# Optimization experiments

Measured on AMD Instinct MI355X. Metric: run time of the kernel, lower is better.

Reference implementation:

```python
import jax, jax.numpy as jnp
import numpy as np

N, F_IN, HID, HEADS, NC, E, NG = 50000, 128, 64, 4, 8, 800000, 512


def setup_inputs() -> dict:
    key = jax.random.key(0)
    ks = jax.random.split(key, 16)
    x = jax.random.normal(ks[0], (N, F_IN), dtype=jnp.float32)
    # edges with src != dst so every node's incoming set is exactly {neighbors, self-loop}
    dst = jax.random.randint(ks[1], (E,), 0, N, dtype=jnp.int64)
    off = jax.random.randint(ks[2], (E,), 1, N, dtype=jnp.int64)
    src = (dst + off) % N
    edge_index = jnp.stack([src, dst])
    batch = jnp.sort(jax.random.randint(ks[3], (N,), 0, NG, dtype=jnp.int64))
    g = 1.0 / np.sqrt(F_IN)
    W1 = jax.random.uniform(ks[4], (F_IN, HEADS * HID), jnp.float32, -g, g)
    att_src1 = jax.random.normal(ks[5], (HEADS, HID), jnp.float32) * 0.1
    att_dst1 = jax.random.normal(ks[6], (HEADS, HID), jnp.float32) * 0.1
    b1 = jnp.zeros((HEADS * HID,), jnp.float32)
    g2 = 1.0 / np.sqrt(HEADS * HID)
    W2 = jax.random.uniform(ks[7], (HEADS * HID, HID), jnp.float32, -g2, g2)
    att_src2 = jax.random.normal(ks[8], (1, HID), jnp.float32) * 0.1
    att_dst2 = jax.random.normal(ks[9], (1, HID), jnp.float32) * 0.1
    b2 = jnp.zeros((HID,), jnp.float32)
    g3 = 1.0 / np.sqrt(HID)
    lin_w = jax.random.uniform(ks[10], (HID, NC), jnp.float32, -g3, g3)
    lin_b = jnp.zeros((NC,), jnp.float32)
    return dict(x=x, edge_index=edge_index, batch=batch, W1=W1, att_src1=att_src1,
                att_dst1=att_dst1, b1=b1, W2=W2, att_src2=att_src2, att_dst2=att_dst2,
                b2=b2, lin_w=lin_w, lin_b=lin_b)


def gat_layer(x, src, dst, W, att_s, att_d, bias, heads, out_ch):
    # PyG GATConv: h = x @ W, e_ij = LeakyReLU(a_s.h_j + a_d.h_i), softmax over dst groups
    h = (x @ W).reshape(-1, heads, out_ch)                    # [N,H,C]
    a_s = jnp.einsum('nhc,hc->nh', h, att_s)                  # [N,H]
    a_d = jnp.einsum('nhc,hc->nh', h, att_d)
    e = jax.nn.leaky_relu(a_s[src] + a_d[dst], 0.2)           # [Ef,H]
    m = jax.ops.segment_max(e, dst, num_segments=N)           # stable segment softmax
    ex = jnp.exp(e - m[dst])
    s = jax.ops.segment_sum(ex, dst, num_segments=N)
    alpha = ex / (s[dst] + 1e-16)                             # [Ef,H]
    msg = h[src] * alpha[:, :, None]                          # [Ef,H,C]
    out = jax.ops.segment_sum(msg, dst, num_segments=N)       # [N,H,C]
    return out.reshape(-1, heads * out_ch) + bias, alpha


def reference(x, edge_index, batch, W1, att_src1, att_dst1, b1,
              W2, att_src2, att_dst2, b2, lin_w, lin_b):
    loops = jnp.arange(N, dtype=edge_index.dtype)
    src = jnp.concatenate([edge_index[0], loops])             # add self-loops (PyG default)
    dst = jnp.concatenate([edge_index[1], loops])
    h, alpha1 = gat_layer(x, src, dst, W1, att_src1, att_dst1, b1, HEADS, HID)
    h = jax.nn.relu(h)
    # conv2 on edge_index_1 (already has self-loops; PyG remove+add is a no-op here)
    h, alpha2 = gat_layer(h, src, dst, W2, att_src2, att_dst2, b2, 1, HID)
    h = jax.nn.relu(h)
    sums = jax.ops.segment_sum(h, batch, num_segments=NG)     # global_mean_pool
    cnt = jax.ops.segment_sum(jnp.ones((N,), h.dtype), batch, num_segments=NG)
    pooled = sums / jnp.maximum(cnt, 1.0)[:, None]
    # dropout is identity in eval mode
    return pooled @ lin_w + lin_b
```

## Files before the change

kernel.cpp:

```cpp
#include <hip/hip_runtime.h>

#define F_IN 128
#define HID 64
#define HEADS 4
#define NC 8

typedef __bf16 bf16_t;
typedef bf16_t bf16x8 __attribute__((ext_vector_type(8)));
typedef float f32x4 __attribute__((ext_vector_type(4)));

union BF8 { bf16x8 v; ushort u[8]; };


__device__ __forceinline__ ushort f2bf(float f) {
    uint u = __float_as_uint(f);
    return (ushort)((u + 0x7fffu + ((u >> 16) & 1u)) >> 16);
}
__device__ __forceinline__ float bf2f(ushort h) {
    return __uint_as_float(((uint)h) << 16);
}
__device__ __forceinline__ float edgew(float e) {
    e = (e > 0.f) ? e : 0.2f * e;
    return __expf(e);
}

__global__ void k_setup(const float* __restrict__ W1, const float* __restrict__ W2,
                        ushort* __restrict__ w1hi, ushort* __restrict__ w1lo,
                        ushort* __restrict__ w2hi, ushort* __restrict__ w2lo,
                        int* __restrict__ deg, int N, int* __restrict__ counts, int NG) {
    int i = blockIdx.x * blockDim.x + threadIdx.x;
    if (i < N) deg[i] = 1;
    if (i < NG) counts[i] = 0;
    if (i < 128 * 256) {
        int k = i >> 8, n = i & 255;
        int cy = n >> 7, ct = (n >> 4) & 7, c = n & 15, kc = k >> 5, ls = (k >> 3) & 3, j = k & 7;
        size_t off = ((((size_t)cy * 8 + ct) * 4 + kc) * 64 + (ls * 16 + c)) * 8 + j;
        float w = W1[i];
        ushort hi = f2bf(w);
        w1hi[off] = hi; w1lo[off] = f2bf(w - bf2f(hi));
    }
    if (i < 256 * 64) {
        int k = i >> 6, n = i & 63;
        int ct = n >> 4, c = n & 15, kc = k >> 5, ls = (k >> 3) & 3, j = k & 7;
        size_t off = (((size_t)ct * 8 + kc) * 64 + (ls * 16 + c)) * 8 + j;
        float w = W2[i];
        ushort hi = f2bf(w);
        w2hi[off] = hi; w2lo[off] = f2bf(w - bf2f(hi));
    }
}

__global__ void k_count(const int* __restrict__ ei, int E, int* __restrict__ deg,
                        const int* __restrict__ batch, int N, int* __restrict__ counts) {
    int i = blockIdx.x * blockDim.x + threadIdx.x;
    if (i < E) atomicAdd(&deg[ei[E + i]], 1);
    if (i < N) atomicAdd(&counts[batch[i]], 1);
}

__global__ __launch_bounds__(1024) void k_scan_part(const int* __restrict__ v,
                                                    int* __restrict__ excl,
                                                    int* __restrict__ bsum, int n) {
    __shared__ int buf[1024];
    int tid = threadIdx.x;
    int i = blockIdx.x * 1024 + tid;
    int val = (i < n) ? v[i] : 0;
    buf[tid] = val;
    __syncthreads();
    for (int off = 1; off < 1024; off <<= 1) {
        int t = (tid >= off) ? buf[tid - off] : 0;
        __syncthreads();
        buf[tid] += t;
        __syncthreads();
    }
    if (i < n) excl[i] = buf[tid] - val;
    if (tid == 1023) bsum[blockIdx.x] = buf[1023];
}

__global__ __launch_bounds__(1024) void k_scan_small2(const int* __restrict__ bsum,
                                                      int* __restrict__ boff, int nb,
                                                      int* __restrict__ total_out,
                                                      const int* __restrict__ counts,
                                                      int* __restrict__ gstart, int ng) {
    __shared__ int buf[1024];
    int tid = threadIdx.x;
    const int* src = (blockIdx.x == 0) ? bsum : counts;
    int cnt = (blockIdx.x == 0) ? nb : ng;
    int val = (tid < cnt) ? src[tid] : 0;
    buf[tid] = val;
    __syncthreads();
    for (int off = 1; off < 1024; off <<= 1) {
        int t = (tid >= off) ? buf[tid - off] : 0;
        __syncthreads();
        buf[tid] += t;
        __syncthreads();
    }
    if (blockIdx.x == 0) {
        if (tid < cnt) boff[tid] = buf[tid] - val;
        if (tid == 1023) total_out[0] = buf[1023];
    } else {
        if (tid < cnt) gstart[tid] = buf[tid] - val;
        if (tid == 1023) gstart[ng] = buf[1023];
    }
}

__global__ void k_scan_add_self(int* __restrict__ rowstart, const int* __restrict__ boff,
                                int* __restrict__ cursor, int* __restrict__ csr, int n) {
    int i = blockIdx.x * blockDim.x + threadIdx.x;
    if (i < n) {
        int rs = rowstart[i] + boff[i >> 10];
        rowstart[i] = rs;
        csr[rs] = i;
        cursor[i] = 1;
    }
}

__global__ void k_scatter(const int* __restrict__ ei, int E, const int* __restrict__ rowstart,
                          int* __restrict__ cursor, int* __restrict__ csr) {
    int e = blockIdx.x * blockDim.x + threadIdx.x;
    if (e < E) {
        int d = ei[E + e], s = ei[e];
        int pos = atomicAdd(&cursor[d], 1);
        csr[rowstart[d] + pos] = s;
    }
}

__global__ __launch_bounds__(256) void k_gemm1(const float* __restrict__ x,
                                               const ushort* __restrict__ w1hi,
                                               const ushort* __restrict__ w1lo,
                                               const float* __restrict__ atts,
                                               const float* __restrict__ attd,
                                               ushort* __restrict__ h1b,
                                               float* __restrict__ as1, float* __restrict__ ad1,
                                               int N) {
    __shared__ __align__(16) ushort lhi[16384];
    __shared__ __align__(16) ushort llo[16384];
    int tid = threadIdx.x;
    int cy = blockIdx.y;
    {
        float4* dh = (float4*)lhi; const float4* sh = (const float4*)(w1hi + (size_t)cy * 16384);
        float4* dl = (float4*)llo; const float4* sl = (const float4*)(w1lo + (size_t)cy * 16384);
        #pragma unroll
        for (int i = 0; i < 8; i++) {
            dh[tid + i * 256] = sh[tid + i * 256];
            dl[tid + i * 256] = sl[tid + i * 256];
        }
    }
    __syncthreads();
    int w = tid >> 6, l = tid & 63;
    int lc = l & 15, lk = l >> 4;
    int rbase = blockIdx.x * 256 + w * 64;

    f32x4 acc[4][8];
    #pragma unroll
    for (int mt = 0; mt < 4; mt++)
        #pragma unroll
        for (int ct = 0; ct < 8; ct++) acc[mt][ct] = (f32x4){0.f, 0.f, 0.f, 0.f};

    #pragma unroll
    for (int kc = 0; kc < 4; kc++) {
        BF8 ahi[4], alo[4];
        #pragma unroll
        for (int mt = 0; mt < 4; mt++) {
            int row = rbase + mt * 16 + lc;
            float4 v0 = {0.f, 0.f, 0.f, 0.f}, v1 = v0;
            if (row < N) {
                const float* xp = x + (size_t)row * F_IN + kc * 32 + lk * 8;
                v0 = *(const float4*)xp; v1 = *(const float4*)(xp + 4);
            }
            float vals[8] = {v0.x, v0.y, v0.z, v0.w, v1.x, v1.y, v1.z, v1.w};
            #pragma unroll
            for (int j = 0; j < 8; j++) {
                ushort h = f2bf(vals[j]);
                ahi[mt].u[j] = h;
                alo[mt].u[j] = f2bf(vals[j] - bf2f(h));
            }
        }
        #pragma unroll
        for (int ct = 0; ct < 8; ct++) {
            int boff = ((ct * 4 + kc) * 64 + l) * 8;
            bf16x8 bhi = *(const bf16x8*)(lhi + boff);
            bf16x8 blo = *(const bf16x8*)(llo + boff);
            #pragma unroll
            for (int mt = 0; mt < 4; mt++) {
                acc[mt][ct] = __builtin_amdgcn_mfma_f32_16x16x32_bf16(ahi[mt].v, bhi, acc[mt][ct], 0, 0, 0);
                acc[mt][ct] = __builtin_amdgcn_mfma_f32_16x16x32_bf16(alo[mt].v, bhi, acc[mt][ct], 0, 0, 0);
                acc[mt][ct] = __builtin_amdgcn_mfma_f32_16x16x32_bf16(ahi[mt].v, blo, acc[mt][ct], 0, 0, 0);
            }
        }
    }
    #pragma unroll
    for (int mt = 0; mt < 4; mt++) {
        int rowb = rbase + mt * 16 + lk * 4;
        #pragma unroll
        for (int ct = 0; ct < 8; ct++) {
            int col = cy * 128 + ct * 16 + lc;
            #pragma unroll
            for (int r = 0; r < 4; r++) {
                int row = rowb + r;
                if (row < N) h1b[(size_t)row * 256 + col] = f2bf(acc[mt][ct][r]);
            }
        }
        #pragma unroll
        for (int hh = 0; hh < 2; hh++) {
            float s[4] = {0.f, 0.f, 0.f, 0.f}, d[4] = {0.f, 0.f, 0.f, 0.f};
            #pragma unroll
            for (int cq = 0; cq < 4; cq++) {
                int ct = hh * 4 + cq;
                int col = cy * 128 + ct * 16 + lc;
                float av = atts[col], dv = attd[col];
                #pragma unroll
                for (int r = 0; r < 4; r++) { s[r] += acc[mt][ct][r] * av; d[r] += acc[mt][ct][r] * dv; }
            }
            #pragma unroll
            for (int r = 0; r < 4; r++) {
                #pragma unroll
                for (int off = 1; off < 16; off <<= 1) {
                    s[r] += __shfl_xor(s[r], off);
                    d[r] += __shfl_xor(d[r], off);
                }
            }
            if (lc == 0) {
                int head = cy * 2 + hh;
                #pragma unroll
                for (int r = 0; r < 4; r++) {
                    int row = rowb + r;
                    if (row < N) { as1[row * 4 + head] = s[r]; ad1[row * 4 + head] = d[r]; }
                }
            }
        }
    }
}

__global__ __launch_bounds__(256) void k_gemm2(const ushort* __restrict__ xin,
                                               const ushort* __restrict__ w2hi,
                                               const ushort* __restrict__ w2lo,
                                               const float* __restrict__ atts,
                                               const float* __restrict__ attd,
                                               ushort* __restrict__ h2b,
                                               float* __restrict__ as2, float* __restrict__ ad2,
                                               int N) {
    __shared__ __align__(16) ushort lhi[16384];
    __shared__ __align__(16) ushort llo[16384];
    int tid = threadIdx.x;
    {
        float4* dh = (float4*)lhi; const float4* sh = (const float4*)w2hi;
        float4* dl = (float4*)llo; const float4* sl = (const float4*)w2lo;
        #pragma unroll
        for (int i = 0; i < 8; i++) {
            dh[tid + i * 256] = sh[tid + i * 256];
            dl[tid + i * 256] = sl[tid + i * 256];
        }
    }
    __syncthreads();
    int w = tid >> 6, l = tid & 63;
    int lc = l & 15, lk = l >> 4;
    int rbase = blockIdx.x * 256 + w * 64;

    f32x4 acc[4][4];
    #pragma unroll
    for (int mt = 0; mt < 4; mt++)
        #pragma unroll
        for (int ct = 0; ct < 4; ct++) acc[mt][ct] = (f32x4){0.f, 0.f, 0.f, 0.f};

    #pragma unroll
    for (int kc = 0; kc < 8; kc++) {
        BF8 a[4];
        #pragma unroll
        for (int mt = 0; mt < 4; mt++) {
            int row = rbase + mt * 16 + lc;
            if (row < N) {
                a[mt].v = *(const bf16x8*)(xin + (size_t)row * 256 + kc * 32 + lk * 8);
            } else {
                #pragma unroll
                for (int j = 0; j < 8; j++) a[mt].u[j] = 0;
            }
        }
        #pragma unroll
        for (int ct = 0; ct < 4; ct++) {
            int boff = ((ct * 8 + kc) * 64 + l) * 8;
            bf16x8 bhi = *(const bf16x8*)(lhi + boff);
            bf16x8 blo = *(const bf16x8*)(llo + boff);
            #pragma unroll
            for (int mt = 0; mt < 4; mt++) {
                acc[mt][ct] = __builtin_amdgcn_mfma_f32_16x16x32_bf16(a[mt].v, bhi, acc[mt][ct], 0, 0, 0);
                acc[mt][ct] = __builtin_amdgcn_mfma_f32_16x16x32_bf16(a[mt].v, blo, acc[mt][ct], 0, 0, 0);
            }
        }
    }
    #pragma unroll
    for (int mt = 0; mt < 4; mt++) {
        int rowb = rbase + mt * 16 + lk * 4;
        #pragma unroll
        for (int ct = 0; ct < 4; ct++) {
            int col = ct * 16 + lc;
            #pragma unroll
            for (int r = 0; r < 4; r++) {
                int row = rowb + r;
                if (row < N) h2b[(size_t)row * 64 + col] = f2bf(acc[mt][ct][r]);
            }
        }
        float s[4] = {0.f, 0.f, 0.f, 0.f}, d[4] = {0.f, 0.f, 0.f, 0.f};
        #pragma unroll
        for (int ct = 0; ct < 4; ct++) {
            int col = ct * 16 + lc;
            float av = atts[col], dv = attd[col];
            #pragma unroll
            for (int r = 0; r < 4; r++) { s[r] += acc[mt][ct][r] * av; d[r] += acc[mt][ct][r] * dv; }
        }
        #pragma unroll
        for (int r = 0; r < 4; r++) {
            #pragma unroll
            for (int off = 1; off < 16; off <<= 1) {
                s[r] += __shfl_xor(s[r], off);
                d[r] += __shfl_xor(d[r], off);
            }
        }
        if (lc == 0) {
            #pragma unroll
            for (int r = 0; r < 4; r++) {
                int row = rowb + r;
                if (row < N) { as2[row] = s[r]; ad2[row] = d[r]; }
            }
        }
    }
}


__global__ __launch_bounds__(256) void k_agg1(const ushort* __restrict__ h1b,
                                              const float* __restrict__ as, const float* __restrict__ ad,
                                              const int* __restrict__ rowstart, const int* __restrict__ csr,
                                              const float* __restrict__ b1,
                                              ushort* __restrict__ out1b, int N) {
    int n = blockIdx.x * 4 + (threadIdx.x >> 6);
    int lane = threadIdx.x & 63;
    if (n >= N) return;
    int head = lane >> 4;
    int coff = lane * 4;
    float adv = ad[n * 4 + head];
    int beg = rowstart[n], end = rowstart[n + 1];
    float a0 = 0.f, a1 = 0.f, a2 = 0.f, a3 = 0.f, ssum = 0.f;
    int j = beg;
    for (; j + 8 <= end; j += 8) {
        int s[8];
        #pragma unroll
        for (int i = 0; i < 8; i++) s[i] = csr[j + i];
        float e[8];
        #pragma unroll
        for (int i = 0; i < 8; i++) e[i] = as[s[i] * 4 + head];
        ushort4 hv[8];
        #pragma unroll
        for (int i = 0; i < 8; i++) hv[i] = *(const ushort4*)(h1b + (size_t)s[i] * 256 + coff);
        #pragma unroll
        for (int i = 0; i < 8; i++) {
            float wv = edgew(e[i] + adv);
            ssum += wv;
            a0 += wv * bf2f(hv[i].x); a1 += wv * bf2f(hv[i].y);
            a2 += wv * bf2f(hv[i].z); a3 += wv * bf2f(hv[i].w);
        }
    }
    for (; j < end; j++) {
        int s0 = csr[j];
        float wv = edgew(as[s0 * 4 + head] + adv);
        ushort4 v0 = *(const ushort4*)(h1b + (size_t)s0 * 256 + coff);
        ssum += wv;
        a0 += wv * bf2f(v0.x); a1 += wv * bf2f(v0.y);
        a2 += wv * bf2f(v0.z); a3 += wv * bf2f(v0.w);
    }
    float inv = 1.f / ssum;
    float o0 = fmaxf(a0 * inv + b1[coff + 0], 0.f);
    float o1 = fmaxf(a1 * inv + b1[coff + 1], 0.f);
    float o2 = fmaxf(a2 * inv + b1[coff + 2], 0.f);
    float o3 = fmaxf(a3 * inv + b1[coff + 3], 0.f);
    ushort4 o;
    o.x = f2bf(o0); o.y = f2bf(o1); o.z = f2bf(o2); o.w = f2bf(o3);
    *(ushort4*)(out1b + (size_t)n * 256 + coff) = o;
}

__global__ __launch_bounds__(256) void k_agg2(const ushort* __restrict__ h2b,
                                              const float* __restrict__ as, const float* __restrict__ ad,
                                              const int* __restrict__ rowstart, const int* __restrict__ csr,
                                              const float* __restrict__ b2,
                                              float* __restrict__ out2, int N) {
    int n = blockIdx.x * 4 + (threadIdx.x >> 6);
    int lane = threadIdx.x & 63;
    if (n >= N) return;
    float adv = ad[n];
    int beg = rowstart[n], end = rowstart[n + 1];
    float acc = 0.f, ssum = 0.f;
    int j = beg;
    for (; j + 8 <= end; j += 8) {
        int s[8];
        #pragma unroll
        for (int i = 0; i < 8; i++) s[i] = csr[j + i];
        float e[8];
        #pragma unroll
        for (int i = 0; i < 8; i++) e[i] = as[s[i]];
        ushort hv[8];
        #pragma unroll
        for (int i = 0; i < 8; i++) hv[i] = h2b[(size_t)s[i] * 64 + lane];
        #pragma unroll
        for (int i = 0; i < 8; i++) {
            float wv = edgew(e[i] + adv);
            ssum += wv;
            acc += wv * bf2f(hv[i]);
        }
    }
    for (; j < end; j++) {
        int s0 = csr[j];
        float wv = edgew(as[s0] + adv);
        ssum += wv;
        acc += wv * bf2f(h2b[(size_t)s0 * 64 + lane]);
    }
    float o = acc / ssum + b2[lane];
    out2[(size_t)n * 64 + lane] = o > 0.f ? o : 0.f;
}


__global__ __launch_bounds__(64) void k_pool(const float* __restrict__ out2,
                                             const int* __restrict__ gstart,
                                             const float* __restrict__ lin_w,
                                             const float* __restrict__ lin_b,
                                             float* __restrict__ out, int NG) {
    __shared__ float mean[64];
    int g = blockIdx.x;
    int lane = threadIdx.x;
    int beg = gstart[g], end = gstart[g + 1];
    float s = 0.f;
    for (int n = beg; n < end; n++) s += out2[(size_t)n * 64 + lane];
    float cnt = (float)(end - beg);
    mean[lane] = s / fmaxf(cnt, 1.f);
    __syncthreads();
    if (lane < NC) {
        float acc = lin_b[lane];
        #pragma unroll
        for (int c = 0; c < 64; c++) acc += mean[c] * lin_w[c * NC + lane];
        out[g * NC + lane] = acc;
    }
}


extern "C" void kernel_launch(void* const* d_in, const int* in_sizes, int n_in,
                              void* d_out, int out_size, void* d_ws, size_t ws_size,
                              hipStream_t stream) {
    const float* x      = (const float*)d_in[0];
    const int*   ei     = (const int*)d_in[1];
    const int*   batch  = (const int*)d_in[2];
    const float* W1     = (const float*)d_in[3];
    const float* att_s1 = (const float*)d_in[4];
    const float* att_d1 = (const float*)d_in[5];
    const float* b1     = (const float*)d_in[6];
    const float* W2     = (const float*)d_in[7];
    const float* att_s2 = (const float*)d_in[8];
    const float* att_d2 = (const float*)d_in[9];
    const float* b2     = (const float*)d_in[10];
    const float* lin_w  = (const float*)d_in[11];
    const float* lin_b  = (const float*)d_in[12];
    float* out = (float*)d_out;

    const int N  = in_sizes[0] / F_IN;
    const int E  = in_sizes[1] / 2;
    const int NG = out_size / NC;
    const int NE = E + N;
    const int NB = (N + 1023) / 1024;

    char* p = (char*)d_ws;
    auto alloc = [&](size_t bytes) { char* r = p; p += (bytes + 255) & ~(size_t)255; return r; };
    ushort* h1b     = (ushort*)alloc(sizeof(ushort) * (size_t)N * 256);
    ushort* out1b   = (ushort*)alloc(sizeof(ushort) * (size_t)N * 256);
    ushort* h2b     = (ushort*)alloc(sizeof(ushort) * (size_t)N * 64);
    float*  out2    = (float*)alloc(sizeof(float) * (size_t)N * 64);
    float*  as1     = (float*)alloc(sizeof(float) * (size_t)N * 4);
    float*  ad1     = (float*)alloc(sizeof(float) * (size_t)N * 4);
    float*  as2     = (float*)alloc(sizeof(float) * (size_t)N);
    float*  ad2     = (float*)alloc(sizeof(float) * (size_t)N);
    int*    rowstart= (int*)alloc(sizeof(int) * (size_t)(N + 1));
    int*    itmp    = (int*)alloc(sizeof(int) * (size_t)N);
    int*    csr     = (int*)alloc(sizeof(int) * (size_t)NE);
    int*    counts  = (int*)alloc(sizeof(int) * (size_t)NG);
    int*    gstart  = (int*)alloc(sizeof(int) * (size_t)(NG + 1));
    int*    bsum    = (int*)alloc(sizeof(int) * 1024);
    int*    boff    = (int*)alloc(sizeof(int) * 1024);
    ushort* w1hi    = (ushort*)alloc(sizeof(ushort) * 32768);
    ushort* w1lo    = (ushort*)alloc(sizeof(ushort) * 32768);
    ushort* w2hi    = (ushort*)alloc(sizeof(ushort) * 16384);
    ushort* w2lo    = (ushort*)alloc(sizeof(ushort) * 16384);

    int bs = 256;
    k_setup<<<(N + bs - 1) / bs, bs, 0, stream>>>(W1, W2, w1hi, w1lo, w2hi, w2lo,
                                                  itmp, N, counts, NG);
    k_count<<<(E + bs - 1) / bs, bs, 0, stream>>>(ei, E, itmp, batch, N, counts);
    k_scan_part<<<NB, 1024, 0, stream>>>(itmp, rowstart, bsum, N);
    k_scan_small2<<<2, 1024, 0, stream>>>(bsum, boff, NB, rowstart + N, counts, gstart, NG);
    k_scan_add_self<<<(N + 1023) / 1024, 1024, 0, stream>>>(rowstart, boff, itmp, csr, N);
    k_scatter<<<(E + bs - 1) / bs, bs, 0, stream>>>(ei, E, rowstart, itmp, csr);

    k_gemm1<<<dim3((N + 255) / 256, 2), 256, 0, stream>>>(x, w1hi, w1lo, att_s1, att_d1, h1b, as1, ad1, N);
    k_agg1<<<(N + 3) / 4, 256, 0, stream>>>(h1b, as1, ad1, rowstart, csr, b1, out1b, N);

    k_gemm2<<<(N + 255) / 256, 256, 0, stream>>>(out1b, w2hi, w2lo, att_s2, att_d2, h2b, as2, ad2, N);
    k_agg2<<<(N + 3) / 4, 256, 0, stream>>>(h2b, as2, ad2, rowstart, csr, b2, out2, N);

    k_pool<<<NG, 64, 0, stream>>>(out2, gstart, lin_w, lin_b, out, NG);
}
```

Baseline: 321.4 us.

## Drop W1 low-part GEMM term and restructure aggregation to edge-parallel staging

Layer-1 GEMM no longer computes the bf16 low-part correction for W1, which removes one of three MFMAs per tile along with half the weight LDS traffic. Both aggregation kernels are rewritten so each wave computes edge weights for 64 edges in parallel, stages them in shared memory, and then gathers neighbour features with 16-byte loads, splitting edges across lane groups and combining the partial sums with shuffles. The aim is more memory-level parallelism and wider loads in the gather-bound aggregation. It costs some GEMM1 accuracy and relies on wave-level implicit synchronisation when reading the shared staging arrays without a barrier.

```diff
diff --git a/kernel.cpp b/kernel.cpp
--- a/kernel.cpp
+++ b/kernel.cpp
@@ -25,7 +25,7 @@
 }
 
 __global__ void k_setup(const float* __restrict__ W1, const float* __restrict__ W2,
-                        ushort* __restrict__ w1hi, ushort* __restrict__ w1lo,
+                        ushort* __restrict__ w1hi,
                         ushort* __restrict__ w2hi, ushort* __restrict__ w2lo,
                         int* __restrict__ deg, int N, int* __restrict__ counts, int NG) {
     int i = blockIdx.x * blockDim.x + threadIdx.x;
@@ -35,9 +35,7 @@
         int k = i >> 8, n = i & 255;
         int cy = n >> 7, ct = (n >> 4) & 7, c = n & 15, kc = k >> 5, ls = (k >> 3) & 3, j = k & 7;
         size_t off = ((((size_t)cy * 8 + ct) * 4 + kc) * 64 + (ls * 16 + c)) * 8 + j;
-        float w = W1[i];
-        ushort hi = f2bf(w);
-        w1hi[off] = hi; w1lo[off] = f2bf(w - bf2f(hi));
+        w1hi[off] = f2bf(W1[i]);
     }
     if (i < 256 * 64) {
         int k = i >> 6, n = i & 63;
@@ -125,24 +123,18 @@
 
 __global__ __launch_bounds__(256) void k_gemm1(const float* __restrict__ x,
                                                const ushort* __restrict__ w1hi,
-                                               const ushort* __restrict__ w1lo,
                                                const float* __restrict__ atts,
                                                const float* __restrict__ attd,
                                                ushort* __restrict__ h1b,
                                                float* __restrict__ as1, float* __restrict__ ad1,
                                                int N) {
     __shared__ __align__(16) ushort lhi[16384];
-    __shared__ __align__(16) ushort llo[16384];
     int tid = threadIdx.x;
     int cy = blockIdx.y;
     {
         float4* dh = (float4*)lhi; const float4* sh = (const float4*)(w1hi + (size_t)cy * 16384);
-        float4* dl = (float4*)llo; const float4* sl = (const float4*)(w1lo + (size_t)cy * 16384);
-        #pragma unroll
-        for (int i = 0; i < 8; i++) {
-            dh[tid + i * 256] = sh[tid + i * 256];
-            dl[tid + i * 256] = sl[tid + i * 256];
-        }
+        #pragma unroll
+        for (int i = 0; i < 8; i++) dh[tid + i * 256] = sh[tid + i * 256];
     }
     __syncthreads();
     int w = tid >> 6, l = tid & 63;
@@ -178,12 +170,10 @@
         for (int ct = 0; ct < 8; ct++) {
             int boff = ((ct * 4 + kc) * 64 + l) * 8;
             bf16x8 bhi = *(const bf16x8*)(lhi + boff);
-            bf16x8 blo = *(const bf16x8*)(llo + boff);
             #pragma unroll
             for (int mt = 0; mt < 4; mt++) {
                 acc[mt][ct] = __builtin_amdgcn_mfma_f32_16x16x32_bf16(ahi[mt].v, bhi, acc[mt][ct], 0, 0, 0);
                 acc[mt][ct] = __builtin_amdgcn_mfma_f32_16x16x32_bf16(alo[mt].v, bhi, acc[mt][ct], 0, 0, 0);
-                acc[mt][ct] = __builtin_amdgcn_mfma_f32_16x16x32_bf16(ahi[mt].v, blo, acc[mt][ct], 0, 0, 0);
             }
         }
     }
@@ -324,94 +314,165 @@
     }
 }
 
-
-__global__ __launch_bounds__(256) void k_agg1(const ushort* __restrict__ h1b,
-                                              const float* __restrict__ as, const float* __restrict__ ad,
-                                              const int* __restrict__ rowstart, const int* __restrict__ csr,
-                                              const float* __restrict__ b1,
-                                              ushort* __restrict__ out1b, int N) {
-    int n = blockIdx.x * 4 + (threadIdx.x >> 6);
-    int lane = threadIdx.x & 63;
+__global__ __launch_bounds__(256) void k_fagg1(const ushort* __restrict__ h1b,
+                                               const float* __restrict__ as1,
+                                               const float* __restrict__ ad1,
+                                               const int* __restrict__ rowstart,
+                                               const int* __restrict__ csr,
+                                               const float* __restrict__ b1,
+                                               ushort* __restrict__ out1b, int N) {
+    __shared__ float lw[4][256];
+    __shared__ int   lsrc[4][64];
+    int wid = threadIdx.x >> 6, lane = threadIdx.x & 63;
+    int n = blockIdx.x * 4 + wid;
     if (n >= N) return;
-    int head = lane >> 4;
-    int coff = lane * 4;
-    float adv = ad[n * 4 + head];
     int beg = rowstart[n], end = rowstart[n + 1];
-    float a0 = 0.f, a1 = 0.f, a2 = 0.f, a3 = 0.f, ssum = 0.f;
-    int j = beg;
-    for (; j + 8 <= end; j += 8) {
-        int s[8];
-        #pragma unroll
-        for (int i = 0; i < 8; i++) s[i] = csr[j + i];
-        float e[8];
-        #pragma unroll
-        for (int i = 0; i < 8; i++) e[i] = as[s[i] * 4 + head];
-        ushort4 hv[8];
-        #pragma unroll
-        for (int i = 0; i < 8; i++) hv[i] = *(const ushort4*)(h1b + (size_t)s[i] * 256 + coff);
-        #pragma unroll
-        for (int i = 0; i < 8; i++) {
-            float wv = edgew(e[i] + adv);
-            ssum += wv;
-            a0 += wv * bf2f(hv[i].x); a1 += wv * bf2f(hv[i].y);
-            a2 += wv * bf2f(hv[i].z); a3 += wv * bf2f(hv[i].w);
-        }
-    }
-    for (; j < end; j++) {
-        int s0 = csr[j];
-        float wv = edgew(as[s0 * 4 + head] + adv);
-        ushort4 v0 = *(const ushort4*)(h1b + (size_t)s0 * 256 + coff);
-        ssum += wv;
-        a0 += wv * bf2f(v0.x); a1 += wv * bf2f(v0.y);
-        a2 += wv * bf2f(v0.z); a3 += wv * bf2f(v0.w);
-    }
-    float inv = 1.f / ssum;
-    float o0 = fmaxf(a0 * inv + b1[coff + 0], 0.f);
-    float o1 = fmaxf(a1 * inv + b1[coff + 1], 0.f);
-    float o2 = fmaxf(a2 * inv + b1[coff + 2], 0.f);
-    float o3 = fmaxf(a3 * inv + b1[coff + 3], 0.f);
-    ushort4 o;
-    o.x = f2bf(o0); o.y = f2bf(o1); o.z = f2bf(o2); o.w = f2bf(o3);
-    *(ushort4*)(out1b + (size_t)n * 256 + coff) = o;
-}
-
-__global__ __launch_bounds__(256) void k_agg2(const ushort* __restrict__ h2b,
-                                              const float* __restrict__ as, const float* __restrict__ ad,
-                                              const int* __restrict__ rowstart, const int* __restrict__ csr,
-                                              const float* __restrict__ b2,
-                                              float* __restrict__ out2, int N) {
-    int n = blockIdx.x * 4 + (threadIdx.x >> 6);
-    int lane = threadIdx.x & 63;
+    float4 adv = *(const float4*)(ad1 + (size_t)n * 4);
+    int lh = lane & 31, half = lane >> 5;
+    int c0 = lh * 8;
+    int head = lh >> 3;
+    float s0 = 0.f, s1 = 0.f, s2 = 0.f, s3 = 0.f;
+    float a[8];
+    #pragma unroll
+    for (int i = 0; i < 8; i++) a[i] = 0.f;
+
+    for (int jc = beg; jc < end; jc += 64) {
+        int j = jc + lane;
+        float4 wv = {0.f, 0.f, 0.f, 0.f};
+        int src = 0;
+        if (j < end) {
+            src = csr[j];
+            float4 av = *(const float4*)(as1 + (size_t)src * 4);
+            wv.x = edgew(av.x + adv.x); wv.y = edgew(av.y + adv.y);
+            wv.z = edgew(av.z + adv.z); wv.w = edgew(av.w + adv.w);
+            s0 += wv.x; s1 += wv.y; s2 += wv.z; s3 += wv.w;
+        }
+        *(float4*)&lw[wid][lane * 4] = wv;
+        lsrc[wid][lane] = src;
+        int cnt = min(64, end - jc);
+        int pairs = (cnt + 1) >> 1;
+        for (int t = 0; t < pairs; t += 4) {
+            #pragma unroll
+            for (int u = 0; u < 4; u++) {
+                int tt = t + u;
+                if (tt < pairs) {
+                    int e = 2 * tt + half;
+                    int sr = lsrc[wid][e];
+                    float wgt = lw[wid][e * 4 + head];
+                    uint4 hv = *(const uint4*)(h1b + (size_t)sr * 256 + c0);
+                    a[0] += wgt * bf2f((ushort)(hv.x & 0xffffu));
+                    a[1] += wgt * bf2f((ushort)(hv.x >> 16));
+                    a[2] += wgt * bf2f((ushort)(hv.y & 0xffffu));
+                    a[3] += wgt * bf2f((ushort)(hv.y >> 16));
+                    a[4] += wgt * bf2f((ushort)(hv.z & 0xffffu));
+                    a[5] += wgt * bf2f((ushort)(hv.z >> 16));
+                    a[6] += wgt * bf2f((ushort)(hv.w & 0xffffu));
+                    a[7] += wgt * bf2f((ushort)(hv.w >> 16));
+                }
+            }
+        }
+    }
+    #pragma unroll
+    for (int i = 0; i < 8; i++) a[i] += __shfl_xor(a[i], 32);
+    #pragma unroll
+    for (int off = 1; off < 64; off <<= 1) {
+        s0 += __shfl_xor(s0, off); s1 += __shfl_xor(s1, off);
+        s2 += __shfl_xor(s2, off); s3 += __shfl_xor(s3, off);
+    }
+    float sv = (head == 0) ? s0 : (head == 1) ? s1 : (head == 2) ? s2 : s3;
+    float inv = 1.f / sv;
+    if (half == 0) {
+        const float4* bv = (const float4*)(b1 + c0);
+        float4 bA = bv[0], bB = bv[1];
+        float o0 = fmaxf(a[0] * inv + bA.x, 0.f), o1 = fmaxf(a[1] * inv + bA.y, 0.f);
+        float o2 = fmaxf(a[2] * inv + bA.z, 0.f), o3 = fmaxf(a[3] * inv + bA.w, 0.f);
+        float o4 = fmaxf(a[4] * inv + bB.x, 0.f), o5 = fmaxf(a[5] * inv + bB.y, 0.f);
+        float o6 = fmaxf(a[6] * inv + bB.z, 0.f), o7 = fmaxf(a[7] * inv + bB.w, 0.f);
+        uint4 ov;
+        ov.x = (uint)f2bf(o0) | ((uint)f2bf(o1) << 16);
+        ov.y = (uint)f2bf(o2) | ((uint)f2bf(o3) << 16);
+        ov.z = (uint)f2bf(o4) | ((uint)f2bf(o5) << 16);
+        ov.w = (uint)f2bf(o6) | ((uint)f2bf(o7) << 16);
+        *(uint4*)(out1b + (size_t)n * 256 + c0) = ov;
+    }
+}
+
+__global__ __launch_bounds__(256) void k_fagg2(const ushort* __restrict__ h2b,
+                                               const float* __restrict__ as2,
+                                               const float* __restrict__ ad2,
+                                               const int* __restrict__ rowstart,
+                                               const int* __restrict__ csr,
+                                               const float* __restrict__ b2,
+                                               float* __restrict__ out2, int N) {
+    __shared__ float lw[4][64];
+    __shared__ int   lsrc[4][64];
+    int wid = threadIdx.x >> 6, lane = threadIdx.x & 63;
+    int n = blockIdx.x * 4 + wid;
     if (n >= N) return;
-    float adv = ad[n];
     int beg = rowstart[n], end = rowstart[n + 1];
-    float acc = 0.f, ssum = 0.f;
-    int j = beg;
-    for (; j + 8 <= end; j += 8) {
-        int s[8];
-        #pragma unroll
-        for (int i = 0; i < 8; i++) s[i] = csr[j + i];
-        float e[8];
-        #pragma unroll
-        for (int i = 0; i < 8; i++) e[i] = as[s[i]];
-        ushort hv[8];
-        #pragma unroll
-        for (int i = 0; i < 8; i++) hv[i] = h2b[(size_t)s[i] * 64 + lane];
-        #pragma unroll
-        for (int i = 0; i < 8; i++) {
-            float wv = edgew(e[i] + adv);
-            ssum += wv;
-            acc += wv * bf2f(hv[i]);
-        }
-    }
-    for (; j < end; j++) {
-        int s0 = csr[j];
-        float wv = edgew(as[s0] + adv);
-        ssum += wv;
-        acc += wv * bf2f(h2b[(size_t)s0 * 64 + lane]);
-    }
-    float o = acc / ssum + b2[lane];
-    out2[(size_t)n * 64 + lane] = o > 0.f ? o : 0.f;
+    float adv = ad2[n];
+    int g = lane >> 3, li = lane & 7;
+    int c0 = li * 8;
+    float ss = 0.f;
+    float a[8];
+    #pragma unroll
+    for (int i = 0; i < 8; i++) a[i] = 0.f;
+
+    for (int jc = beg; jc < end; jc += 64) {
+        int j = jc + lane;
+        float wgt = 0.f;
+        int src = 0;
+        if (j < end) {
+            src = csr[j];
+            wgt = edgew(as2[src] + adv);
+            ss += wgt;
+        }
+        lw[wid][lane] = wgt;
+        lsrc[wid][lane] = src;
+        int cnt = min(64, end - jc);
+        int groups = (cnt + 7) >> 3;
+        for (int t = 0; t < groups; t += 2) {
+            #pragma unroll
+            for (int u = 0; u < 2; u++) {
+                int tt = t + u;
+                if (tt < groups) {
+                    int e = tt * 8 + g;
+                    int sr = lsrc[wid][e];
+                    float wv = lw[wid][e];
+                    uint4 hv = *(const uint4*)(h2b + (size_t)sr * 64 + c0);
+                    a[0] += wv * bf2f((ushort)(hv.x & 0xffffu));
+                    a[1] += wv * bf2f((ushort)(hv.x >> 16));
+                    a[2] += wv * bf2f((ushort)(hv.y & 0xffffu));
+                    a[3] += wv * bf2f((ushort)(hv.y >> 16));
+                    a[4] += wv * bf2f((ushort)(hv.z & 0xffffu));
+                    a[5] += wv * bf2f((ushort)(hv.z >> 16));
+                    a[6] += wv * bf2f((ushort)(hv.w & 0xffffu));
+                    a[7] += wv * bf2f((ushort)(hv.w >> 16));
+                }
+            }
+        }
+    }
+    #pragma unroll
+    for (int i = 0; i < 8; i++) {
+        a[i] += __shfl_xor(a[i], 8);
+        a[i] += __shfl_xor(a[i], 16);
+        a[i] += __shfl_xor(a[i], 32);
+    }
+    #pragma unroll
+    for (int off = 1; off < 64; off <<= 1) ss += __shfl_xor(ss, off);
+    float inv = 1.f / ss;
+    if (g == 0) {
+        const float4* bv = (const float4*)(b2 + c0);
+        float4 bA = bv[0], bB = bv[1];
+        float4 oA, oB;
+        oA.x = fmaxf(a[0] * inv + bA.x, 0.f); oA.y = fmaxf(a[1] * inv + bA.y, 0.f);
+        oA.z = fmaxf(a[2] * inv + bA.z, 0.f); oA.w = fmaxf(a[3] * inv + bA.w, 0.f);
+        oB.x = fmaxf(a[4] * inv + bB.x, 0.f); oB.y = fmaxf(a[5] * inv + bB.y, 0.f);
+        oB.z = fmaxf(a[6] * inv + bB.z, 0.f); oB.w = fmaxf(a[7] * inv + bB.w, 0.f);
+        float* op = out2 + (size_t)n * 64 + c0;
+        *(float4*)op = oA;
+        *(float4*)(op + 4) = oB;
+    }
 }
 
 
@@ -480,12 +541,11 @@
     int*    bsum    = (int*)alloc(sizeof(int) * 1024);
     int*    boff    = (int*)alloc(sizeof(int) * 1024);
     ushort* w1hi    = (ushort*)alloc(sizeof(ushort) * 32768);
-    ushort* w1lo    = (ushort*)alloc(sizeof(ushort) * 32768);
     ushort* w2hi    = (ushort*)alloc(sizeof(ushort) * 16384);
     ushort* w2lo    = (ushort*)alloc(sizeof(ushort) * 16384);
 
     int bs = 256;
-    k_setup<<<(N + bs - 1) / bs, bs, 0, stream>>>(W1, W2, w1hi, w1lo, w2hi, w2lo,
+    k_setup<<<(N + bs - 1) / bs, bs, 0, stream>>>(W1, W2, w1hi, w2hi, w2lo,
                                                   itmp, N, counts, NG);
     k_count<<<(E + bs - 1) / bs, bs, 0, stream>>>(ei, E, itmp, batch, N, counts);
     k_scan_part<<<NB, 1024, 0, stream>>>(itmp, rowstart, bsum, N);
@@ -493,11 +553,11 @@
     k_scan_add_self<<<(N + 1023) / 1024, 1024, 0, stream>>>(rowstart, boff, itmp, csr, N);
     k_scatter<<<(E + bs - 1) / bs, bs, 0, stream>>>(ei, E, rowstart, itmp, csr);
 
-    k_gemm1<<<dim3((N + 255) / 256, 2), 256, 0, stream>>>(x, w1hi, w1lo, att_s1, att_d1, h1b, as1, ad1, N);
-    k_agg1<<<(N + 3) / 4, 256, 0, stream>>>(h1b, as1, ad1, rowstart, csr, b1, out1b, N);
+    k_gemm1<<<dim3((N + 255) / 256, 2), 256, 0, stream>>>(x, w1hi, att_s1, att_d1, h1b, as1, ad1, N);
+    k_fagg1<<<(N + 3) / 4, 256, 0, stream>>>(h1b, as1, ad1, rowstart, csr, b1, out1b, N);
 
     k_gemm2<<<(N + 255) / 256, 256, 0, stream>>>(out1b, w2hi, w2lo, att_s2, att_d2, h2b, as2, ad2, N);
-    k_agg2<<<(N + 3) / 4, 256, 0, stream>>>(h2b, as2, ad2, rowstart, csr, b2, out2, N);
+    k_fagg2<<<(N + 3) / 4, 256, 0, stream>>>(h2b, as2, ad2, rowstart, csr, b2, out2, N);
 
     k_pool<<<NG, 64, 0, stream>>>(out2, gstart, lin_w, lin_b, out, NG);
 }
```

Result: faster. 305.4 us (-5.0%).
